# Performance work log

Hardware: AMD Instinct MI355X
Metric: run time of the kernel (lower is better)

The kernel has to match this reference:

```python
import jax, jax.numpy as jnp
import numpy as np

B, N, HIST, PRED, KHOP, H = 64, 1085, 24, 24, 3, 64
FX, FM = 1, 11
F = FX + FM  # node feature dim fed to gnn (12)
E = 17360


def setup_inputs() -> dict:
    key = jax.random.key(0)
    ks = jax.random.split(key, 13)
    s = 0.1
    return {
        "x_hist": jax.random.normal(ks[0], (B, HIST, N, FX), jnp.float32),
        "enc_misc": jax.random.normal(ks[1], (B, HIST, N, FM), jnp.float32),
        "dec": jax.random.normal(ks[2], (B, PRED, N, FM), jnp.float32),
        "We": jax.random.normal(ks[3], (2 * F, F), jnp.float32) * s,
        "be": jnp.zeros((F,), jnp.float32),
        "Wx": jax.random.normal(ks[4], (KHOP, 2 * F, 3 * H), jnp.float32) * s,
        "Wh": jax.random.normal(ks[5], (KHOP, H, 3 * H), jnp.float32) * s,
        "bx": jnp.zeros((KHOP, 3 * H), jnp.float32),
        "bh": jnp.zeros((KHOP, 3 * H), jnp.float32),
        "fc_w": jax.random.normal(ks[6], (KHOP * H, FX), jnp.float32) * s,
        "fc_b": jnp.zeros((FX,), jnp.float32),
        "src": jax.random.randint(ks[7], (E,), 0, N, jnp.int32),
        "dst": jax.random.randint(ks[8], (E,), 0, N, jnp.int32),
    }


def reference(x_hist, enc_misc, dec, We, be, Wx, Wh, bx, bh, fc_w, fc_b, src, dst):
    features = jnp.concatenate([enc_misc, dec], axis=1)  # (B, HIST+PRED, N, FM)

    def gnn(x):  # x: (B, N, F) -> (B, N, F); edge MLP + scatter-sum + residual
        m = jax.nn.relu(jnp.concatenate([x[:, src], x[:, dst]], -1) @ We + be)  # (B,E,F)
        return x + jnp.zeros_like(x).at[:, dst].add(m)

    def gru(x, h, k):  # x: (B*N, 2F), h: (B*N, H)
        g = x @ Wx[k] + bx[k]
        gh = h @ Wh[k] + bh[k]
        r = jax.nn.sigmoid(g[:, :H] + gh[:, :H])
        z = jax.nn.sigmoid(g[:, H:2 * H] + gh[:, H:2 * H])
        n = jnp.tanh(g[:, 2 * H:] + r * gh[:, 2 * H:])
        return (1.0 - z) * n + z * h

    def run_step(hn, xn):  # xn: (B, N, F)
        xg = xn
        new = list(hn)
        for k in range(KHOP):
            xg = gnn(xg)
            x_gru = jnp.concatenate([xg, xn], -1).reshape(B * N, 2 * F)
            new[k] = gru(x_gru, new[k], k)
        return tuple(new)

    h0 = tuple(jnp.zeros((B * N, H), x_hist.dtype) for _ in range(KHOP))

    def hist_step(hn, inp):
        xp, ft = inp  # (B,N,FX), (B,N,FM)
        return run_step(hn, jnp.concatenate([xp, ft], -1)), None

    hist_xs = (jnp.swapaxes(x_hist[:, :HIST - 1], 0, 1),
               jnp.swapaxes(features[:, 1:HIST], 0, 1))
    hn, _ = jax.lax.scan(hist_step, h0, hist_xs)

    def pred_step(carry, ft):
        hn, x = carry
        hn = run_step(hn, jnp.concatenate([x, ft], -1))
        hn_all = jnp.concatenate([h.reshape(B, N, H) for h in hn], -1)  # (B,N,KHOP*H)
        x_new = hn_all @ fc_w + fc_b  # (B, N, FX)
        return (hn, x_new), x_new

    _, ys = jax.lax.scan(pred_step, (hn, x_hist[:, -1]),
                         jnp.swapaxes(features[:, HIST:], 0, 1))
    return jnp.swapaxes(ys, 0, 1)  # (B, PRED, N, FX)
```

## Files before the change

kernel.cpp:

```cpp
#include <hip/hip_runtime.h>

#define NB 64
#define NNODE 1085
#define HIST 24
#define PRED 24
#define KHOP 3
#define HDIM 64
#define FXD 1
#define FMD 11
#define FD 12
#define NE 17360
#define NROWS (NB*NNODE)
#define WPAR 1024


typedef float v4 __attribute__((ext_vector_type(4)));

__device__ __forceinline__ float sigm(float x){ return 1.0f/(1.0f + __expf(-x)); }
__device__ __forceinline__ float tanh_f(float x){ return 1.0f - 2.0f/(__expf(2.0f*x)+1.0f); }

__global__ void csr_count_k(const int* __restrict__ dst, int* __restrict__ deg)
{
    int e = blockIdx.x*256 + threadIdx.x;
    if (e < NE) atomicAdd(&deg[dst[e]], 1);
}

__global__ __launch_bounds__(1024) void csr_scan_k(const int* __restrict__ deg,
                                                   int* __restrict__ offs, int* __restrict__ curs)
{
    __shared__ int s[2][2048];
    int t = threadIdx.x;
    for (int i=t;i<2048;i+=1024) s[0][i] = (i<NNODE) ? deg[i] : 0;
    __syncthreads();
    int cur = 0;
    for (int d=1; d<2048; d<<=1){
        for (int i=t;i<2048;i+=1024){
            int v = s[cur][i];
            if (i>=d) v += s[cur][i-d];
            s[cur^1][i] = v;
        }
        __syncthreads();
        cur ^= 1;
    }
    for (int i=t;i<=NNODE;i+=1024){
        int v = (i==0) ? 0 : s[cur][i-1];
        offs[i] = v;
        if (i<NNODE) curs[i] = v;
    }
}

__global__ void csr_fill_k(const int* __restrict__ dst, const int* __restrict__ src,
                           int* __restrict__ curs, int* __restrict__ esrc)
{
    int e = blockIdx.x*256 + threadIdx.x;
    if (e < NE){
        int d = dst[e];
        int p = atomicAdd(&curs[d], 1);
        esrc[p] = src[e];
    }
}

__global__ void csr_part_k(const int* __restrict__ offs, int* __restrict__ wpart)
{
    int w = blockIdx.x*256 + threadIdx.x;
    if (w > WPAR) return;
    if (w == 0)    { wpart[0] = 0;        return; }
    if (w == WPAR) { wpart[WPAR] = NNODE; return; }
    int target = (int)(((long)w * NE) / WPAR);
    int lo = 0, hi = NNODE;
    while (lo < hi){ int mid = (lo+hi)>>1; if (offs[mid] >= target) hi = mid; else lo = mid+1; }
    wpart[w] = lo;
}

__global__ void build_hist_k(const float* __restrict__ x_hist, const float* __restrict__ enc_misc,
                             int t0, int T, float* __restrict__ xn_all)
{
    long idx = (long)blockIdx.x*256 + threadIdx.x;
    if (idx >= (long)T*NROWS) return;
    int b = (int)(idx & 63);
    long nn = idx >> 6;
    int ti = (int)(nn / NNODE);
    int n  = (int)(nn - (long)ti*NNODE);
    int t  = t0 + ti;
    float* xp = xn_all + (long)ti*NROWS*FD + (long)n*FD*64 + b;
    xp[0] = x_hist[((long)b*HIST + t)*NNODE + n];
    const float* fp = enc_misc + (((long)b*HIST + (t+1))*NNODE + n)*FMD;
    #pragma unroll
    for (int i=0;i<FMD;i++) xp[(1+i)*64] = fp[i];
}

__global__ void build_xn_k(const float* __restrict__ xsrc, int from_xcur,
                           const float* __restrict__ dec, int p,
                           float* __restrict__ xn)
{
    int idx = blockIdx.x*256 + threadIdx.x;
    if (idx >= NROWS) return;
    int b = idx & 63, n = idx >> 6;
    float v0 = from_xcur ? xsrc[idx]
                         : xsrc[((long)b*HIST + (HIST-1))*NNODE + n];
    float* xp = xn + (long)n*FD*64 + b;
    xp[0] = v0;
    const float* fp = dec + (((long)b*PRED + p)*NNODE + n)*FMD;
    #pragma unroll
    for (int i=0;i<FMD;i++) xp[(1+i)*64] = fp[i];
}

__global__ __launch_bounds__(256) void gnn_gather_k(const float* __restrict__ xin,
    const float* __restrict__ We, const float* __restrict__ be,
    const int* __restrict__ esrc, const int* __restrict__ offs,
    const int* __restrict__ wpart, float* __restrict__ xout)
{
    __shared__ float w_s[288];
    __shared__ float be_s[12];
    const int tid = threadIdx.x;
    for (int i=tid;i<288;i+=256) w_s[i]=We[i];
    if (tid<12) be_s[tid]=be[tid];
    __syncthreads();

    const int lane = tid & 63;
    const int wave = (blockIdx.x*256 + tid) >> 6;
    const long sbase = (long)blockIdx.y * ((long)NROWS*FD);
    const float* x = xin + sbase;
    float* xo = xout + sbase;

    const int n0 = wpart[wave], n1 = wpart[wave+1];
    for (int n=n0; n<n1; ++n){
        float xd[12], part[12], acc[12];
        const float* xb = x + (long)n*768 + lane;
        #pragma unroll
        for (int f=0;f<12;f++) xd[f] = xb[f*64];
        #pragma unroll
        for (int f=0;f<12;f++){ part[f]=be_s[f]; acc[f]=0.f; }
        #pragma unroll
        for (int f=0;f<12;f++){
            float xv = xd[f];
            const float* wrow = &w_s[(12+f)*12];
            #pragma unroll
            for (int j=0;j<12;j++) part[j] += xv*wrow[j];
        }
        const int e0 = offs[n], e1 = offs[n+1];
        for (int idx=e0; idx<e1; ++idx){
            int s = esrc[idx];
            const float* xsb = x + (long)s*768 + lane;
            float m[12];
            #pragma unroll
            for (int f=0;f<12;f++) m[f]=part[f];
            #pragma unroll
            for (int f=0;f<12;f++){
                float xv = xsb[f*64];
                const float* wrow = &w_s[f*12];
                #pragma unroll
                for (int j=0;j<12;j++) m[j] += xv*wrow[j];
            }
            #pragma unroll
            for (int f=0;f<12;f++) acc[f] += fmaxf(m[f],0.f);
        }
        float* xob = xo + (long)n*768 + lane;
        #pragma unroll
        for (int f=0;f<12;f++) xob[f*64] = xd[f] + acc[f];
    }
}

#define KC 44
__global__ __launch_bounds__(256) void gru3_k(
    const float* __restrict__ xg_base, long k_stride,
    const float* __restrict__ xn,
    float* __restrict__ h_base,
    const float* __restrict__ Wx, const float* __restrict__ Wh,
    const float* __restrict__ bx, const float* __restrict__ bh)
{
    const int k = blockIdx.y;
    const int n = blockIdx.x;
    const float* xgn = xg_base + (long)k*k_stride + (long)n*768;
    const float* xnn = xn + (long)n*768;
    float*       hn  = h_base + ((size_t)k*NROWS + (long)n*64)*HDIM;
    const float* wx  = Wx + (size_t)k*24*192;
    const float* wh  = Wh + (size_t)k*64*192;
    const float* bxk = bx + k*192;
    const float* bhk = bh + k*192;

    __shared__ __align__(16) float A_s[KC][64];
    __shared__ __align__(16) float W_s[KC][192];
    const int tid = threadIdx.x;
    const int tx = tid & 15, ty = tid >> 4;

    const v4* wx4 = (const v4*)wx;
    const v4* wh4 = (const v4*)wh;
    const v4* h4  = (const v4*)hn;

    float acc_r[16], acc_z[16], acc_gn[16], acc_ghn[16];
    #pragma unroll
    for (int i=0;i<16;i++){ acc_r[i]=0.f; acc_z[i]=0.f; acc_gn[i]=0.f; acc_ghn[i]=0.f; }

    for (int i=tid; i<KC*48; i+=256){
        int kk = i/48, q = i - kk*48;
        v4 w = (kk<24) ? wx4[kk*48+q] : wh4[(kk-24)*48+q];
        *(v4*)&W_s[kk][q*4] = w;
    }
    for (int i=tid; i<192; i+=256) ((v4*)A_s)[i]       = ((const v4*)xgn)[i];
    for (int i=tid; i<192; i+=256) ((v4*)A_s)[192+i]   = ((const v4*)xnn)[i];
    for (int i=tid; i<320; i+=256){
        int r = i/5, q = i - r*5;
        v4 v = h4[r*16+q];
        #pragma unroll
        for (int j=0;j<4;j++) A_s[24+4*q+j][r] = v[j];
    }
    __syncthreads();
    #pragma unroll 4
    for (int kk=0;kk<24;kk++){
        v4 av=*(const v4*)&A_s[kk][ty*4];
        v4 wr=*(const v4*)&W_s[kk][tx*4];
        v4 wz=*(const v4*)&W_s[kk][64+tx*4];
        v4 wn=*(const v4*)&W_s[kk][128+tx*4];
        #pragma unroll
        for (int dr=0;dr<4;dr++)
            #pragma unroll
            for (int dc=0;dc<4;dc++){
                acc_r[dr*4+dc]+=av[dr]*wr[dc];
                acc_z[dr*4+dc]+=av[dr]*wz[dc];
                acc_gn[dr*4+dc]+=av[dr]*wn[dc];
            }
    }
    #pragma unroll 4
    for (int kk=24;kk<44;kk++){
        v4 av=*(const v4*)&A_s[kk][ty*4];
        v4 wr=*(const v4*)&W_s[kk][tx*4];
        v4 wz=*(const v4*)&W_s[kk][64+tx*4];
        v4 wn=*(const v4*)&W_s[kk][128+tx*4];
        #pragma unroll
        for (int dr=0;dr<4;dr++)
            #pragma unroll
            for (int dc=0;dc<4;dc++){
                acc_r[dr*4+dc]+=av[dr]*wr[dc];
                acc_z[dr*4+dc]+=av[dr]*wz[dc];
                acc_ghn[dr*4+dc]+=av[dr]*wn[dc];
            }
    }
    __syncthreads();
    for (int i=tid; i<KC*48; i+=256){
        int kk = i/48, q = i - kk*48;
        *(v4*)&W_s[kk][q*4] = wh4[(20+kk)*48+q];
    }
    for (int i=tid; i<704; i+=256){
        int r = i/11, q = i - r*11;
        v4 v = h4[r*16+5+q];
        #pragma unroll
        for (int j=0;j<4;j++) A_s[4*q+j][r] = v[j];
    }
    __syncthreads();
    #pragma unroll 4
    for (int kk=0;kk<44;kk++){
        v4 av=*(const v4*)&A_s[kk][ty*4];
        v4 wr=*(const v4*)&W_s[kk][tx*4];
        v4 wz=*(const v4*)&W_s[kk][64+tx*4];
        v4 wn=*(const v4*)&W_s[kk][128+tx*4];
        #pragma unroll
        for (int dr=0;dr<4;dr++)
            #pragma unroll
            for (int dc=0;dc<4;dc++){
                acc_r[dr*4+dc]+=av[dr]*wr[dc];
                acc_z[dr*4+dc]+=av[dr]*wz[dc];
                acc_ghn[dr*4+dc]+=av[dr]*wn[dc];
            }
    }

    v4 bxr=*(const v4*)&bxk[tx*4],     bhr=*(const v4*)&bhk[tx*4];
    v4 bxz=*(const v4*)&bxk[64+tx*4],  bhz=*(const v4*)&bhk[64+tx*4];
    v4 bxn=*(const v4*)&bxk[128+tx*4], bhn=*(const v4*)&bhk[128+tx*4];
    #pragma unroll
    for (int dr=0;dr<4;dr++){
        int lr = ty*4 + dr;
        v4 hold = *(const v4*)&hn[lr*HDIM + tx*4];
        v4 hnew;
        #pragma unroll
        for (int dc=0;dc<4;dc++){
            float rr = sigm(acc_r[dr*4+dc] + bxr[dc] + bhr[dc]);
            float zz = sigm(acc_z[dr*4+dc] + bxz[dc] + bhz[dc]);
            float nn = tanh_f(acc_gn[dr*4+dc] + bxn[dc] + rr*(acc_ghn[dr*4+dc] + bhn[dc]));
            hnew[dc] = (1.0f-zz)*nn + zz*hold[dc];
        }
        *(v4*)&hn[lr*HDIM + tx*4] = hnew;
    }
}

__global__ void fc_k(const float* __restrict__ h, const float* __restrict__ fc_w,
                     const float* __restrict__ fc_b, float* __restrict__ x_cur,
                     float* __restrict__ out, int p)
{
    int idx = blockIdx.x*256+threadIdx.x;
    if (idx>=NROWS) return;
    float acc = fc_b[0];
    #pragma unroll
    for (int k=0;k<3;k++){
        const float* hb = h + ((size_t)k*NROWS + idx)*HDIM;
        const float* wb = fc_w + k*HDIM;
        #pragma unroll
        for (int q=0;q<16;q++){
            v4 hv=*(const v4*)&hb[q*4];
            v4 wv=*(const v4*)&wb[q*4];
            acc += hv[0]*wv[0]+hv[1]*wv[1]+hv[2]*wv[2]+hv[3]*wv[3];
        }
    }
    x_cur[idx]=acc;
    int b = idx & 63, n = idx >> 6;
    out[((long)b*PRED + p)*NNODE + n] = acc;
}

extern "C" void kernel_launch(void* const* d_in, const int* in_sizes, int n_in,
                              void* d_out, int out_size, void* d_ws, size_t ws_size,
                              hipStream_t stream)
{
    const float* x_hist   = (const float*)d_in[0];
    const float* enc_misc = (const float*)d_in[1];
    const float* dec      = (const float*)d_in[2];
    const float* We       = (const float*)d_in[3];
    const float* be       = (const float*)d_in[4];
    const float* Wx       = (const float*)d_in[5];
    const float* Wh       = (const float*)d_in[6];
    const float* bx       = (const float*)d_in[7];
    const float* bh       = (const float*)d_in[8];
    const float* fc_w     = (const float*)d_in[9];
    const float* fc_b     = (const float*)d_in[10];
    const int*   src      = (const int*)d_in[11];
    const int*   dst      = (const int*)d_in[12];
    float* out = (float*)d_out;

    const size_t SZ_T = (size_t)NROWS*FD;
    size_t fixed_f = (size_t)3*NROWS*HDIM + NROWS + 64*1024;
    size_t avail_f = ws_size/4;
    long tc = 1;
    if (avail_f > fixed_f + 4*SZ_T)
        tc = (long)((avail_f - fixed_f) / (4*SZ_T));
    if (tc > HIST-1) tc = HIST-1;
    if (tc < 1) tc = 1;
    const long T_CHUNK = tc;

    float* h      = (float*)d_ws;
    float* x_cur  = h + (size_t)3*NROWS*HDIM;
    int*   deg    = (int*)(x_cur + NROWS);
    int*   offs   = deg + NNODE;
    int*   curs   = offs + NNODE + 1;
    int*   wpart  = curs + NNODE;
    int*   esrc   = wpart + WPAR + 1;
    float* xn_all = (float*)(esrc + NE) + 16;
    xn_all = (float*)(((size_t)xn_all + 255) & ~(size_t)255);
    float* xg_all = xn_all + T_CHUNK*SZ_T;
    const long K_STRIDE = T_CHUNK*SZ_T;

    hipMemsetAsync(h, 0, (size_t)3*NROWS*HDIM*sizeof(float), stream);
    hipMemsetAsync(deg, 0, NNODE*sizeof(int), stream);

    const int gE = (NE+255)/256;
    csr_count_k<<<gE,256,0,stream>>>(dst, deg);
    csr_scan_k<<<1,1024,0,stream>>>(deg, offs, curs);
    csr_fill_k<<<gE,256,0,stream>>>(dst, src, curs, esrc);
    csr_part_k<<<(WPAR+256)/256,256,0,stream>>>(offs, wpart);

    const int gRow = (NROWS+255)/256;
    const int gGx  = WPAR*64/256;

    for (int t0 = 0; t0 < HIST-1; t0 += (int)T_CHUNK){
        int T = min((int)T_CHUNK, HIST-1-t0);
        build_hist_k<<<(int)(((long)T*NROWS+255)/256),256,0,stream>>>(x_hist, enc_misc, t0, T, xn_all);
        dim3 gG(gGx, T);
        gnn_gather_k<<<gG,256,0,stream>>>(xn_all,            We,be,esrc,offs,wpart, xg_all);
        gnn_gather_k<<<gG,256,0,stream>>>(xg_all,            We,be,esrc,offs,wpart, xg_all+K_STRIDE);
        gnn_gather_k<<<gG,256,0,stream>>>(xg_all+K_STRIDE,   We,be,esrc,offs,wpart, xg_all+2*K_STRIDE);
        for (int ti=0; ti<T; ti++){
            dim3 gU(NNODE, 3);
            gru3_k<<<gU,256,0,stream>>>(xg_all + ti*SZ_T, K_STRIDE,
                                        xn_all + ti*SZ_T, h, Wx, Wh, bx, bh);
        }
    }

    for (int p=0;p<PRED;p++){
        if (p==0)
            build_xn_k<<<gRow,256,0,stream>>>(x_hist, 0, dec, p, xn_all);
        else
            build_xn_k<<<gRow,256,0,stream>>>(x_cur, 1, dec, p, xn_all);
        dim3 gG(gGx, 1);
        gnn_gather_k<<<gG,256,0,stream>>>(xn_all,          We,be,esrc,offs,wpart, xg_all);
        gnn_gather_k<<<gG,256,0,stream>>>(xg_all,          We,be,esrc,offs,wpart, xg_all+K_STRIDE);
        gnn_gather_k<<<gG,256,0,stream>>>(xg_all+K_STRIDE, We,be,esrc,offs,wpart, xg_all+2*K_STRIDE);
        dim3 gU(NNODE, 3);
        gru3_k<<<gU,256,0,stream>>>(xg_all, K_STRIDE, xn_all, h, Wx, Wh, bx, bh);
        fc_k<<<gRow,256,0,stream>>>(h, fc_w, fc_b, x_cur, out, p);
    }
}
```

Before: 13.63 ms.

## Fuse whole recurrence into one persistent cooperative kernel with grid syncs

Replaces the per-step launch sequence (gather x3, GRU, fc, build_xn) with a single cooperative persistent kernel of 504 or 252 blocks that steps through all history and prediction timesteps, separated by grid.sync barriers. Each third of the blocks handles one hop's GRU over a contiguous node range, and the fc output plus next-step input build are fused into the prediction loop. This removes thousands of kernel launches and the timestep-batched gather. In exchange it gives up the batched-timestep parallelism of the old history gathers and runs at a fixed, much smaller grid, so fewer waves are available to hide memory latency in the gather and GRU work. The GRU also reloads its weights into shared memory for every node.

Measured after the change: 26.39 ms. 93.6% more time.

```diff
diff --git a/kernel.cpp b/kernel.cpp
--- a/kernel.cpp
+++ b/kernel.cpp
@@ -1,17 +1,20 @@
 #include <hip/hip_runtime.h>
+#include <hip/hip_cooperative_groups.h>
+namespace cg = cooperative_groups;
 
 #define NB 64
 #define NNODE 1085
 #define HIST 24
 #define PRED 24
-#define KHOP 3
 #define HDIM 64
-#define FXD 1
 #define FMD 11
 #define FD 12
 #define NE 17360
 #define NROWS (NB*NNODE)
-#define WPAR 1024
+#define GBLK2 504
+#define GBLK1 252
+#define NWAVE_MAX (GBLK2*4)
+#define SZT ((long)NROWS*FD)
 
 
 typedef float v4 __attribute__((ext_vector_type(4)));
@@ -60,250 +63,260 @@
     }
 }
 
-__global__ void csr_part_k(const int* __restrict__ offs, int* __restrict__ wpart)
+__global__ void csr_part_k(const int* __restrict__ offs, int* __restrict__ wpart, int npart)
 {
     int w = blockIdx.x*256 + threadIdx.x;
-    if (w > WPAR) return;
-    if (w == 0)    { wpart[0] = 0;        return; }
-    if (w == WPAR) { wpart[WPAR] = NNODE; return; }
-    int target = (int)(((long)w * NE) / WPAR);
+    if (w > npart) return;
+    if (w == 0)     { wpart[0] = 0;         return; }
+    if (w == npart) { wpart[npart] = NNODE; return; }
+    int target = (int)(((long)w * NE) / npart);
     int lo = 0, hi = NNODE;
     while (lo < hi){ int mid = (lo+hi)>>1; if (offs[mid] >= target) hi = mid; else lo = mid+1; }
     wpart[w] = lo;
 }
 
 __global__ void build_hist_k(const float* __restrict__ x_hist, const float* __restrict__ enc_misc,
-                             int t0, int T, float* __restrict__ xn_all)
+                             float* __restrict__ xn_hist)
 {
     long idx = (long)blockIdx.x*256 + threadIdx.x;
-    if (idx >= (long)T*NROWS) return;
+    if (idx >= (long)(HIST-1)*NROWS) return;
     int b = (int)(idx & 63);
     long nn = idx >> 6;
     int ti = (int)(nn / NNODE);
     int n  = (int)(nn - (long)ti*NNODE);
-    int t  = t0 + ti;
-    float* xp = xn_all + (long)ti*NROWS*FD + (long)n*FD*64 + b;
-    xp[0] = x_hist[((long)b*HIST + t)*NNODE + n];
-    const float* fp = enc_misc + (((long)b*HIST + (t+1))*NNODE + n)*FMD;
+    float* xp = xn_hist + (long)ti*SZT + (long)n*FD*64 + b;
+    xp[0] = x_hist[((long)b*HIST + ti)*NNODE + n];
+    const float* fp = enc_misc + (((long)b*HIST + (ti+1))*NNODE + n)*FMD;
     #pragma unroll
     for (int i=0;i<FMD;i++) xp[(1+i)*64] = fp[i];
 }
 
-__global__ void build_xn_k(const float* __restrict__ xsrc, int from_xcur,
-                           const float* __restrict__ dec, int p,
-                           float* __restrict__ xn)
-{
-    int idx = blockIdx.x*256 + threadIdx.x;
-    if (idx >= NROWS) return;
-    int b = idx & 63, n = idx >> 6;
-    float v0 = from_xcur ? xsrc[idx]
-                         : xsrc[((long)b*HIST + (HIST-1))*NNODE + n];
-    float* xp = xn + (long)n*FD*64 + b;
-    xp[0] = v0;
-    const float* fp = dec + (((long)b*PRED + p)*NNODE + n)*FMD;
-    #pragma unroll
-    for (int i=0;i<FMD;i++) xp[(1+i)*64] = fp[i];
-}
-
-__global__ __launch_bounds__(256) void gnn_gather_k(const float* __restrict__ xin,
+__global__ __launch_bounds__(256,2) void coop_k(
+    const float* __restrict__ x_hist, const float* __restrict__ dec,
+    float* __restrict__ xn_hist, float* __restrict__ xnp,
+    float* __restrict__ xga, float* __restrict__ xgb, float* __restrict__ xgc,
+    float* __restrict__ h,
+    const float* __restrict__ Wx, const float* __restrict__ Wh,
+    const float* __restrict__ bx, const float* __restrict__ bh,
+    const float* __restrict__ fc_w, const float* __restrict__ fc_b,
     const float* __restrict__ We, const float* __restrict__ be,
     const int* __restrict__ esrc, const int* __restrict__ offs,
-    const int* __restrict__ wpart, float* __restrict__ xout)
-{
-    __shared__ float w_s[288];
-    __shared__ float be_s[12];
+    const int* __restrict__ wpart, float* __restrict__ out)
+{
+    __shared__ __align__(16) float W_s[44][192];
+    __shared__ __align__(16) float A_s[44][64];
+    __shared__ float wg_s[288];
+    __shared__ float beg_s[12];
+
+    cg::grid_group grid = cg::this_grid();
     const int tid = threadIdx.x;
-    for (int i=tid;i<288;i+=256) w_s[i]=We[i];
-    if (tid<12) be_s[tid]=be[tid];
+    const int bph  = gridDim.x/3;
+    const int hop  = blockIdx.x / bph;
+    const int hidx = blockIdx.x - hop*bph;
+    const int nn0 = (hidx*NNODE)/bph, nn1 = ((hidx+1)*NNODE)/bph;
+    const int tx = tid & 15, ty = tid >> 4;
+    const int lane = tid & 63;
+    const int wave = blockIdx.x*4 + (tid>>6);
+
+    for (int i=tid;i<288;i+=256) wg_s[i]=We[i];
+    if (tid<12) beg_s[tid]=be[tid];
     __syncthreads();
 
-    const int lane = tid & 63;
-    const int wave = (blockIdx.x*256 + tid) >> 6;
-    const long sbase = (long)blockIdx.y * ((long)NROWS*FD);
-    const float* x = xin + sbase;
-    float* xo = xout + sbase;
-
-    const int n0 = wpart[wave], n1 = wpart[wave+1];
-    for (int n=n0; n<n1; ++n){
-        float xd[12], part[12], acc[12];
-        const float* xb = x + (long)n*768 + lane;
+    const v4* wx4 = (const v4*)(Wx + (size_t)hop*24*192);
+    const v4* wh4 = (const v4*)(Wh + (size_t)hop*64*192);
+    const float* bxk = bx + hop*192;
+    const float* bhk = bh + hop*192;
+
+    auto gather_phase = [&](const float* __restrict__ x, float* __restrict__ xo){
+        const int n0 = wpart[wave], n1 = wpart[wave+1];
+        for (int n=n0; n<n1; ++n){
+            float xd[12], part[12], acc[12];
+            const float* xb = x + (long)n*768 + lane;
+            #pragma unroll
+            for (int f=0;f<12;f++) xd[f] = xb[f*64];
+            #pragma unroll
+            for (int f=0;f<12;f++){ part[f]=beg_s[f]; acc[f]=0.f; }
+            #pragma unroll
+            for (int f=0;f<12;f++){
+                float xv = xd[f];
+                const float* wrow = &wg_s[(12+f)*12];
+                #pragma unroll
+                for (int j=0;j<12;j++) part[j] += xv*wrow[j];
+            }
+            const int e0 = offs[n], e1 = offs[n+1];
+            for (int idx=e0; idx<e1; ++idx){
+                int s2 = esrc[idx];
+                const float* xsb = x + (long)s2*768 + lane;
+                float m[12];
+                #pragma unroll
+                for (int f=0;f<12;f++) m[f]=part[f];
+                #pragma unroll
+                for (int f=0;f<12;f++){
+                    float xv = xsb[f*64];
+                    const float* wrow = &wg_s[f*12];
+                    #pragma unroll
+                    for (int j=0;j<12;j++) m[j] += xv*wrow[j];
+                }
+                #pragma unroll
+                for (int f=0;f<12;f++) acc[f] += fmaxf(m[f],0.f);
+            }
+            float* xob = xo + (long)n*768 + lane;
+            #pragma unroll
+            for (int f=0;f<12;f++) xob[f*64] = xd[f] + acc[f];
+        }
+    };
+
+    auto gru_phase = [&](const float* __restrict__ xgsl, const float* __restrict__ xnsl){
+        v4 bxr=*(const v4*)&bxk[tx*4],     bhr=*(const v4*)&bhk[tx*4];
+        v4 bxz=*(const v4*)&bxk[64+tx*4],  bhz=*(const v4*)&bhk[64+tx*4];
+        v4 bxn=*(const v4*)&bxk[128+tx*4], bhn=*(const v4*)&bhk[128+tx*4];
+        for (int n=nn0; n<nn1; ++n){
+            const v4* xg4 = (const v4*)(xgsl + (long)n*768);
+            const v4* xn4 = (const v4*)(xnsl + (long)n*768);
+            float* hn = h + ((size_t)hop*NROWS + (long)n*64)*HDIM;
+            const v4* h4 = (const v4*)hn;
+            float ar[16], az[16], agn[16], agh[16];
+            #pragma unroll
+            for (int i=0;i<16;i++){ ar[i]=0.f; az[i]=0.f; agn[i]=0.f; agh[i]=0.f; }
+
+            __syncthreads();
+            for (int i=tid; i<44*48; i+=256){
+                int kk = i/48, q = i - kk*48;
+                *(v4*)&W_s[kk][q*4] = (kk<24) ? wx4[kk*48+q] : wh4[(kk-24)*48+q];
+            }
+            for (int i=tid; i<192; i+=256) ((v4*)A_s)[i]     = xg4[i];
+            for (int i=tid; i<192; i+=256) ((v4*)A_s)[192+i] = xn4[i];
+            for (int i=tid; i<320; i+=256){
+                int r = i/5, q = i - r*5;
+                v4 v = h4[r*16+q];
+                #pragma unroll
+                for (int j=0;j<4;j++) A_s[24+4*q+j][r] = v[j];
+            }
+            __syncthreads();
+            #pragma unroll 4
+            for (int kk=0;kk<24;kk++){
+                v4 av=*(const v4*)&A_s[kk][ty*4];
+                v4 wr=*(const v4*)&W_s[kk][tx*4];
+                v4 wz=*(const v4*)&W_s[kk][64+tx*4];
+                v4 wn=*(const v4*)&W_s[kk][128+tx*4];
+                #pragma unroll
+                for (int dr=0;dr<4;dr++)
+                    #pragma unroll
+                    for (int dc=0;dc<4;dc++){
+                        ar[dr*4+dc]+=av[dr]*wr[dc];
+                        az[dr*4+dc]+=av[dr]*wz[dc];
+                        agn[dr*4+dc]+=av[dr]*wn[dc];
+                    }
+            }
+            #pragma unroll 4
+            for (int kk=24;kk<44;kk++){
+                v4 av=*(const v4*)&A_s[kk][ty*4];
+                v4 wr=*(const v4*)&W_s[kk][tx*4];
+                v4 wz=*(const v4*)&W_s[kk][64+tx*4];
+                v4 wn=*(const v4*)&W_s[kk][128+tx*4];
+                #pragma unroll
+                for (int dr=0;dr<4;dr++)
+                    #pragma unroll
+                    for (int dc=0;dc<4;dc++){
+                        ar[dr*4+dc]+=av[dr]*wr[dc];
+                        az[dr*4+dc]+=av[dr]*wz[dc];
+                        agh[dr*4+dc]+=av[dr]*wn[dc];
+                    }
+            }
+            __syncthreads();
+            for (int i=tid; i<44*48; i+=256){
+                int kk = i/48, q = i - kk*48;
+                *(v4*)&W_s[kk][q*4] = wh4[(20+kk)*48+q];
+            }
+            for (int i=tid; i<704; i+=256){
+                int r = i/11, q = i - r*11;
+                v4 v = h4[r*16+5+q];
+                #pragma unroll
+                for (int j=0;j<4;j++) A_s[4*q+j][r] = v[j];
+            }
+            __syncthreads();
+            #pragma unroll 4
+            for (int kk=0;kk<44;kk++){
+                v4 av=*(const v4*)&A_s[kk][ty*4];
+                v4 wr=*(const v4*)&W_s[kk][tx*4];
+                v4 wz=*(const v4*)&W_s[kk][64+tx*4];
+                v4 wn=*(const v4*)&W_s[kk][128+tx*4];
+                #pragma unroll
+                for (int dr=0;dr<4;dr++)
+                    #pragma unroll
+                    for (int dc=0;dc<4;dc++){
+                        ar[dr*4+dc]+=av[dr]*wr[dc];
+                        az[dr*4+dc]+=av[dr]*wz[dc];
+                        agh[dr*4+dc]+=av[dr]*wn[dc];
+                    }
+            }
+            #pragma unroll
+            for (int dr=0;dr<4;dr++){
+                int lr = ty*4 + dr;
+                v4 hold = *(const v4*)&hn[lr*HDIM + tx*4];
+                v4 hnew;
+                #pragma unroll
+                for (int dc=0;dc<4;dc++){
+                    float rr = sigm(ar[dr*4+dc] + bxr[dc] + bhr[dc]);
+                    float zz = sigm(az[dr*4+dc] + bxz[dc] + bhz[dc]);
+                    float nn2 = tanh_f(agn[dr*4+dc] + bxn[dc] + rr*(agh[dr*4+dc] + bhn[dc]));
+                    hnew[dc] = (1.0f-zz)*nn2 + zz*hold[dc];
+                }
+                *(v4*)&hn[lr*HDIM + tx*4] = hnew;
+            }
+        }
+    };
+
+    for (int t=0; t<HIST-1; ++t){
+        const float* xns = xn_hist + (long)t*SZT;
+        gather_phase(xns, xga);  grid.sync();
+        gather_phase(xga, xgb);  grid.sync();
+        gather_phase(xgb, xgc);  grid.sync();
+        gru_phase(hop==0 ? xga : (hop==1 ? xgb : xgc), xns);
+        grid.sync();
+    }
+
+    for (long idx = (long)blockIdx.x*256 + tid; idx < NROWS; idx += (long)gridDim.x*256){
+        int b = (int)(idx & 63), n = (int)(idx >> 6);
+        float* xp = xnp + (long)n*768 + b;
+        xp[0] = x_hist[((long)b*HIST + (HIST-1))*NNODE + n];
+        const float* fp = dec + (((long)b*PRED + 0)*NNODE + n)*FMD;
         #pragma unroll
-        for (int f=0;f<12;f++) xd[f] = xb[f*64];
-        #pragma unroll
-        for (int f=0;f<12;f++){ part[f]=be_s[f]; acc[f]=0.f; }
-        #pragma unroll
-        for (int f=0;f<12;f++){
-            float xv = xd[f];
-            const float* wrow = &w_s[(12+f)*12];
-            #pragma unroll
-            for (int j=0;j<12;j++) part[j] += xv*wrow[j];
+        for (int i=0;i<FMD;i++) xp[(1+i)*64] = fp[i];
+    }
+    grid.sync();
+
+    for (int p=0; p<PRED; ++p){
+        gather_phase(xnp, xga);  grid.sync();
+        gather_phase(xga, xgb);  grid.sync();
+        gather_phase(xgb, xgc);  grid.sync();
+        gru_phase(hop==0 ? xga : (hop==1 ? xgb : xgc), xnp);
+        grid.sync();
+        for (long idx = (long)blockIdx.x*256 + tid; idx < NROWS; idx += (long)gridDim.x*256){
+            float acc = fc_b[0];
+            #pragma unroll
+            for (int k=0;k<3;k++){
+                const float* hb = h + ((size_t)k*NROWS + idx)*HDIM;
+                const float* wb = fc_w + k*HDIM;
+                #pragma unroll
+                for (int q=0;q<16;q++){
+                    v4 hv=*(const v4*)&hb[q*4];
+                    v4 wv=*(const v4*)&wb[q*4];
+                    acc += hv[0]*wv[0]+hv[1]*wv[1]+hv[2]*wv[2]+hv[3]*wv[3];
+                }
+            }
+            int b = (int)(idx & 63), n = (int)(idx >> 6);
+            out[((long)b*PRED + p)*NNODE + n] = acc;
+            if (p < PRED-1){
+                float* xp = xnp + (long)n*768 + b;
+                xp[0] = acc;
+                const float* fp = dec + (((long)b*PRED + (p+1))*NNODE + n)*FMD;
+                #pragma unroll
+                for (int i=0;i<FMD;i++) xp[(1+i)*64] = fp[i];
+            }
         }
-        const int e0 = offs[n], e1 = offs[n+1];
-        for (int idx=e0; idx<e1; ++idx){
-            int s = esrc[idx];
-            const float* xsb = x + (long)s*768 + lane;
-            float m[12];
-            #pragma unroll
-            for (int f=0;f<12;f++) m[f]=part[f];
-            #pragma unroll
-            for (int f=0;f<12;f++){
-                float xv = xsb[f*64];
-                const float* wrow = &w_s[f*12];
-                #pragma unroll
-                for (int j=0;j<12;j++) m[j] += xv*wrow[j];
-            }
-            #pragma unroll
-            for (int f=0;f<12;f++) acc[f] += fmaxf(m[f],0.f);
-        }
-        float* xob = xo + (long)n*768 + lane;
-        #pragma unroll
-        for (int f=0;f<12;f++) xob[f*64] = xd[f] + acc[f];
-    }
-}
-
-#define KC 44
-__global__ __launch_bounds__(256) void gru3_k(
-    const float* __restrict__ xg_base, long k_stride,
-    const float* __restrict__ xn,
-    float* __restrict__ h_base,
-    const float* __restrict__ Wx, const float* __restrict__ Wh,
-    const float* __restrict__ bx, const float* __restrict__ bh)
-{
-    const int k = blockIdx.y;
-    const int n = blockIdx.x;
-    const float* xgn = xg_base + (long)k*k_stride + (long)n*768;
-    const float* xnn = xn + (long)n*768;
-    float*       hn  = h_base + ((size_t)k*NROWS + (long)n*64)*HDIM;
-    const float* wx  = Wx + (size_t)k*24*192;
-    const float* wh  = Wh + (size_t)k*64*192;
-    const float* bxk = bx + k*192;
-    const float* bhk = bh + k*192;
-
-    __shared__ __align__(16) float A_s[KC][64];
-    __shared__ __align__(16) float W_s[KC][192];
-    const int tid = threadIdx.x;
-    const int tx = tid & 15, ty = tid >> 4;
-
-    const v4* wx4 = (const v4*)wx;
-    const v4* wh4 = (const v4*)wh;
-    const v4* h4  = (const v4*)hn;
-
-    float acc_r[16], acc_z[16], acc_gn[16], acc_ghn[16];
-    #pragma unroll
-    for (int i=0;i<16;i++){ acc_r[i]=0.f; acc_z[i]=0.f; acc_gn[i]=0.f; acc_ghn[i]=0.f; }
-
-    for (int i=tid; i<KC*48; i+=256){
-        int kk = i/48, q = i - kk*48;
-        v4 w = (kk<24) ? wx4[kk*48+q] : wh4[(kk-24)*48+q];
-        *(v4*)&W_s[kk][q*4] = w;
-    }
-    for (int i=tid; i<192; i+=256) ((v4*)A_s)[i]       = ((const v4*)xgn)[i];
-    for (int i=tid; i<192; i+=256) ((v4*)A_s)[192+i]   = ((const v4*)xnn)[i];
-    for (int i=tid; i<320; i+=256){
-        int r = i/5, q = i - r*5;
-        v4 v = h4[r*16+q];
-        #pragma unroll
-        for (int j=0;j<4;j++) A_s[24+4*q+j][r] = v[j];
-    }
-    __syncthreads();
-    #pragma unroll 4
-    for (int kk=0;kk<24;kk++){
-        v4 av=*(const v4*)&A_s[kk][ty*4];
-        v4 wr=*(const v4*)&W_s[kk][tx*4];
-        v4 wz=*(const v4*)&W_s[kk][64+tx*4];
-        v4 wn=*(const v4*)&W_s[kk][128+tx*4];
-        #pragma unroll
-        for (int dr=0;dr<4;dr++)
-            #pragma unroll
-            for (int dc=0;dc<4;dc++){
-                acc_r[dr*4+dc]+=av[dr]*wr[dc];
-                acc_z[dr*4+dc]+=av[dr]*wz[dc];
-                acc_gn[dr*4+dc]+=av[dr]*wn[dc];
-            }
-    }
-    #pragma unroll 4
-    for (int kk=24;kk<44;kk++){
-        v4 av=*(const v4*)&A_s[kk][ty*4];
-        v4 wr=*(const v4*)&W_s[kk][tx*4];
-        v4 wz=*(const v4*)&W_s[kk][64+tx*4];
-        v4 wn=*(const v4*)&W_s[kk][128+tx*4];
-        #pragma unroll
-        for (int dr=0;dr<4;dr++)
-            #pragma unroll
-            for (int dc=0;dc<4;dc++){
-                acc_r[dr*4+dc]+=av[dr]*wr[dc];
-                acc_z[dr*4+dc]+=av[dr]*wz[dc];
-                acc_ghn[dr*4+dc]+=av[dr]*wn[dc];
-            }
-    }
-    __syncthreads();
-    for (int i=tid; i<KC*48; i+=256){
-        int kk = i/48, q = i - kk*48;
-        *(v4*)&W_s[kk][q*4] = wh4[(20+kk)*48+q];
-    }
-    for (int i=tid; i<704; i+=256){
-        int r = i/11, q = i - r*11;
-        v4 v = h4[r*16+5+q];
-        #pragma unroll
-        for (int j=0;j<4;j++) A_s[4*q+j][r] = v[j];
-    }
-    __syncthreads();
-    #pragma unroll 4
-    for (int kk=0;kk<44;kk++){
-        v4 av=*(const v4*)&A_s[kk][ty*4];
-        v4 wr=*(const v4*)&W_s[kk][tx*4];
-        v4 wz=*(const v4*)&W_s[kk][64+tx*4];
-        v4 wn=*(const v4*)&W_s[kk][128+tx*4];
-        #pragma unroll
-        for (int dr=0;dr<4;dr++)
-            #pragma unroll
-            for (int dc=0;dc<4;dc++){
-                acc_r[dr*4+dc]+=av[dr]*wr[dc];
-                acc_z[dr*4+dc]+=av[dr]*wz[dc];
-                acc_ghn[dr*4+dc]+=av[dr]*wn[dc];
-            }
-    }
-
-    v4 bxr=*(const v4*)&bxk[tx*4],     bhr=*(const v4*)&bhk[tx*4];
-    v4 bxz=*(const v4*)&bxk[64+tx*4],  bhz=*(const v4*)&bhk[64+tx*4];
-    v4 bxn=*(const v4*)&bxk[128+tx*4], bhn=*(const v4*)&bhk[128+tx*4];
-    #pragma unroll
-    for (int dr=0;dr<4;dr++){
-        int lr = ty*4 + dr;
-        v4 hold = *(const v4*)&hn[lr*HDIM + tx*4];
-        v4 hnew;
-        #pragma unroll
-        for (int dc=0;dc<4;dc++){
-            float rr = sigm(acc_r[dr*4+dc] + bxr[dc] + bhr[dc]);
-            float zz = sigm(acc_z[dr*4+dc] + bxz[dc] + bhz[dc]);
-            float nn = tanh_f(acc_gn[dr*4+dc] + bxn[dc] + rr*(acc_ghn[dr*4+dc] + bhn[dc]));
-            hnew[dc] = (1.0f-zz)*nn + zz*hold[dc];
-        }
-        *(v4*)&hn[lr*HDIM + tx*4] = hnew;
-    }
-}
-
-__global__ void fc_k(const float* __restrict__ h, const float* __restrict__ fc_w,
-                     const float* __restrict__ fc_b, float* __restrict__ x_cur,
-                     float* __restrict__ out, int p)
-{
-    int idx = blockIdx.x*256+threadIdx.x;
-    if (idx>=NROWS) return;
-    float acc = fc_b[0];
-    #pragma unroll
-    for (int k=0;k<3;k++){
-        const float* hb = h + ((size_t)k*NROWS + idx)*HDIM;
-        const float* wb = fc_w + k*HDIM;
-        #pragma unroll
-        for (int q=0;q<16;q++){
-            v4 hv=*(const v4*)&hb[q*4];
-            v4 wv=*(const v4*)&wb[q*4];
-            acc += hv[0]*wv[0]+hv[1]*wv[1]+hv[2]*wv[2]+hv[3]*wv[3];
-        }
-    }
-    x_cur[idx]=acc;
-    int b = idx & 63, n = idx >> 6;
-    out[((long)b*PRED + p)*NNODE + n] = acc;
+        grid.sync();
+    }
 }
 
 extern "C" void kernel_launch(void* const* d_in, const int* in_sizes, int n_in,
@@ -325,27 +338,23 @@
     const int*   dst      = (const int*)d_in[12];
     float* out = (float*)d_out;
 
-    const size_t SZ_T = (size_t)NROWS*FD;
-    size_t fixed_f = (size_t)3*NROWS*HDIM + NROWS + 64*1024;
-    size_t avail_f = ws_size/4;
-    long tc = 1;
-    if (avail_f > fixed_f + 4*SZ_T)
-        tc = (long)((avail_f - fixed_f) / (4*SZ_T));
-    if (tc > HIST-1) tc = HIST-1;
-    if (tc < 1) tc = 1;
-    const long T_CHUNK = tc;
-
-    float* h      = (float*)d_ws;
-    float* x_cur  = h + (size_t)3*NROWS*HDIM;
-    int*   deg    = (int*)(x_cur + NROWS);
-    int*   offs   = deg + NNODE;
-    int*   curs   = offs + NNODE + 1;
-    int*   wpart  = curs + NNODE;
-    int*   esrc   = wpart + WPAR + 1;
-    float* xn_all = (float*)(esrc + NE) + 16;
-    xn_all = (float*)(((size_t)xn_all + 255) & ~(size_t)255);
-    float* xg_all = xn_all + T_CHUNK*SZ_T;
-    const long K_STRIDE = T_CHUNK*SZ_T;
+    float* h       = (float*)d_ws;
+    float* xn_hist = h + (size_t)3*NROWS*HDIM;
+    float* xnp     = xn_hist + (size_t)(HIST-1)*SZT;
+    float* xga     = xnp + SZT;
+    float* xgb     = xga + SZT;
+    float* xgc     = xgb + SZT;
+    int*   deg     = (int*)(xgc + SZT);
+    int*   offs    = deg + NNODE;
+    int*   curs    = offs + NNODE + 1;
+    int*   wpartC  = curs + NNODE;
+    int*   esrc    = wpartC + NWAVE_MAX + 1;
+
+    int maxB = 0;
+    if (hipOccupancyMaxActiveBlocksPerMultiprocessor(&maxB, coop_k, 256, 0) != hipSuccess || maxB < 1)
+        maxB = 1;
+    const int grid = (maxB >= 2) ? GBLK2 : GBLK1;
+    const int nwave = grid*4;
 
     hipMemsetAsync(h, 0, (size_t)3*NROWS*HDIM*sizeof(float), stream);
     hipMemsetAsync(deg, 0, NNODE*sizeof(int), stream);
@@ -354,36 +363,26 @@
     csr_count_k<<<gE,256,0,stream>>>(dst, deg);
     csr_scan_k<<<1,1024,0,stream>>>(deg, offs, curs);
     csr_fill_k<<<gE,256,0,stream>>>(dst, src, curs, esrc);
-    csr_part_k<<<(WPAR+256)/256,256,0,stream>>>(offs, wpart);
-
-    const int gRow = (NROWS+255)/256;
-    const int gGx  = WPAR*64/256;
-
-    for (int t0 = 0; t0 < HIST-1; t0 += (int)T_CHUNK){
-        int T = min((int)T_CHUNK, HIST-1-t0);
-        build_hist_k<<<(int)(((long)T*NROWS+255)/256),256,0,stream>>>(x_hist, enc_misc, t0, T, xn_all);
-        dim3 gG(gGx, T);
-        gnn_gather_k<<<gG,256,0,stream>>>(xn_all,            We,be,esrc,offs,wpart, xg_all);
-        gnn_gather_k<<<gG,256,0,stream>>>(xg_all,            We,be,esrc,offs,wpart, xg_all+K_STRIDE);
-        gnn_gather_k<<<gG,256,0,stream>>>(xg_all+K_STRIDE,   We,be,esrc,offs,wpart, xg_all+2*K_STRIDE);
-        for (int ti=0; ti<T; ti++){
-            dim3 gU(NNODE, 3);
-            gru3_k<<<gU,256,0,stream>>>(xg_all + ti*SZ_T, K_STRIDE,
-                                        xn_all + ti*SZ_T, h, Wx, Wh, bx, bh);
-        }
-    }
-
-    for (int p=0;p<PRED;p++){
-        if (p==0)
-            build_xn_k<<<gRow,256,0,stream>>>(x_hist, 0, dec, p, xn_all);
-        else
-            build_xn_k<<<gRow,256,0,stream>>>(x_cur, 1, dec, p, xn_all);
-        dim3 gG(gGx, 1);
-        gnn_gather_k<<<gG,256,0,stream>>>(xn_all,          We,be,esrc,offs,wpart, xg_all);
-        gnn_gather_k<<<gG,256,0,stream>>>(xg_all,          We,be,esrc,offs,wpart, xg_all+K_STRIDE);
-        gnn_gather_k<<<gG,256,0,stream>>>(xg_all+K_STRIDE, We,be,esrc,offs,wpart, xg_all+2*K_STRIDE);
-        dim3 gU(NNODE, 3);
-        gru3_k<<<gU,256,0,stream>>>(xg_all, K_STRIDE, xn_all, h, Wx, Wh, bx, bh);
-        fc_k<<<gRow,256,0,stream>>>(h, fc_w, fc_b, x_cur, out, p);
-    }
-}
+    csr_part_k<<<(nwave+256)/256,256,0,stream>>>(offs, wpartC, nwave);
+
+    build_hist_k<<<(int)(((long)(HIST-1)*NROWS+255)/256),256,0,stream>>>(x_hist, enc_misc, xn_hist);
+
+    const float* a_xh = x_hist;  const float* a_dec = dec;
+    float* a_xnh = xn_hist; float* a_xnp = xnp;
+    float* a_xga = xga; float* a_xgb = xgb; float* a_xgc = xgc;
+    float* a_h = h;
+    const float* a_Wx = Wx; const float* a_Wh = Wh;
+    const float* a_bx = bx; const float* a_bh = bh;
+    const float* a_fw = fc_w; const float* a_fb = fc_b;
+    const float* a_We = We; const float* a_be = be;
+    const int* a_es = esrc; const int* a_of = offs; const int* a_wp = wpartC;
+    float* a_out = out;
+    void* args[] = {
+        (void*)&a_xh, (void*)&a_dec, (void*)&a_xnh, (void*)&a_xnp,
+        (void*)&a_xga, (void*)&a_xgb, (void*)&a_xgc, (void*)&a_h,
+        (void*)&a_Wx, (void*)&a_Wh, (void*)&a_bx, (void*)&a_bh,
+        (void*)&a_fw, (void*)&a_fb, (void*)&a_We, (void*)&a_be,
+        (void*)&a_es, (void*)&a_of, (void*)&a_wp, (void*)&a_out
+    };
+    hipLaunchCooperativeKernel((void*)coop_k, dim3(grid), dim3(256), args, 0, stream);
+}
```
